# Kernel tuning notes

Measured on AMD Instinct MI355X. Metric: run time of the kernel, lower is better.

The kernel has to match this reference:

```python
import jax, jax.numpy as jnp
import numpy as np

B, N, NE = 4, 10000, 100000
D, S, H, T = 128, 64, 4, 128      # enc_dim, enc_s_dim, n_head, n_token
NS = D + S                        # GNN node_size = 192
EPS = 1e-5


def linear(x, w, b):
    return x @ w.T + b


def layer_norm(x, g, b):
    m = jnp.mean(x, -1, keepdims=True)
    v = jnp.mean((x - m) ** 2, -1, keepdims=True)
    return (x - m) * jax.lax.rsqrt(v + EPS) * g + b


def mha(q, k, v, wqkv, bqkv, wo, bo):
    # torch nn.MultiheadAttention, batch_first=True
    d = q.shape[-1]; hd = d // H
    wq, wk, wv = jnp.split(wqkv, 3, 0)
    bq, bk, bv = jnp.split(bqkv, 3, 0)
    def proj(x, w, bb):
        Bx, L, _ = x.shape
        return (x @ w.T + bb).reshape(Bx, L, H, hd)
    qh, kh, vh = proj(q, wq, bq), proj(k, wk, bk), proj(v, wv, bv)
    scores = jnp.einsum('bqhd,bkhd->bhqk', qh, kh) / jnp.sqrt(jnp.asarray(hd, q.dtype))
    att = jax.nn.softmax(scores, axis=-1)
    o = jnp.einsum('bhqk,bkhd->bqhd', att, vh).reshape(q.shape[0], q.shape[1], d)
    return o @ wo.T + bo


def smean(vals, idx, n):
    # scatter_mean over one batch element: vals (ne,f), idx (ne,)
    s = jax.ops.segment_sum(vals, idx, num_segments=n)
    c = jax.ops.segment_sum(jnp.ones(idx.shape, vals.dtype), idx, num_segments=n)
    return s / jnp.maximum(c, 1.0)[:, None]

_smean_b = jax.vmap(smean, in_axes=(0, 0, None))
_gather_b = jax.vmap(lambda v, i: v[i])


def setup_inputs():
    key = jax.random.key(0)
    ks = jax.random.split(key, 32)
    r = lambda i, shape: jax.random.normal(ks[i], shape, jnp.float32) * 0.02
    inp = {
        'V': jax.random.normal(ks[0], (B, N, D), jnp.float32),
        'E': jax.random.normal(ks[1], (B, NE, D), jnp.float32),
        'edges': jax.random.randint(ks[2], (B, NE, 2), 0, N),
        's_enc': jax.random.normal(ks[3], (B, N, S), jnp.float32),
        # GNN f_edge: Linear(512,128) SiLU Linear(128,128) LN(128)
        'fe_w1': r(4, (D, D + 2 * NS)), 'fe_b1': jnp.zeros(D),
        'fe_w2': r(5, (D, D)), 'fe_b2': jnp.zeros(D),
        'fe_g': jnp.ones(D), 'fe_be': jnp.zeros(D),
        # GNN f_node: Linear(320,128) SiLU Linear(128,128) LN(128)
        'fn_w1': r(6, (D, NS + D)), 'fn_b1': jnp.zeros(D),
        'fn_w2': r(7, (D, D)), 'fn_b2': jnp.zeros(D),
        'fn_g': jnp.ones(D), 'fn_be': jnp.zeros(D),
        'ln1_g': jnp.ones(D), 'ln1_b': jnp.zeros(D),
        'ln2_g': jnp.ones(D), 'ln2_b': jnp.zeros(D),
        'Q': jax.random.normal(ks[8], (T, D), jnp.float32),
        'a1_wqkv': r(9, (3 * D, D)), 'a1_bqkv': jnp.zeros(3 * D),
        'a1_wo': r(10, (D, D)), 'a1_bo': jnp.zeros(D),
        'a2_wqkv': r(11, (3 * D, D)), 'a2_bqkv': jnp.zeros(3 * D),
        'a2_wo': r(12, (D, D)), 'a2_bo': jnp.zeros(D),
        'a3_wqkv': r(13, (3 * D, D)), 'a3_bqkv': jnp.zeros(3 * D),
        'a3_wo': r(14, (D, D)), 'a3_bo': jnp.zeros(D),
        'ffn_w1': r(15, (2 * D, D)), 'ffn_b1': jnp.zeros(2 * D),
        'ffn_w2': r(16, (D, 2 * D)), 'ffn_b2': jnp.zeros(D),
    }
    return inp


def reference(V, E, edges, s_enc,
              fe_w1, fe_b1, fe_w2, fe_b2, fe_g, fe_be,
              fn_w1, fn_b1, fn_w2, fn_b2, fn_g, fn_be,
              ln1_g, ln1_b, ln2_g, ln2_b,
              Q, a1_wqkv, a1_bqkv, a1_wo, a1_bo,
              a2_wqkv, a2_bqkv, a2_wo, a2_bo,
              a3_wqkv, a3_bqkv, a3_wo, a3_bo,
              ffn_w1, ffn_b1, ffn_w2, ffn_b2):
    n = V.shape[1]
    V_in = jnp.concatenate([V, s_enc], -1)                  # (B,N,192)
    valid = jnp.all(edges >= 0, -1)                          # (B,NE)
    safe = jnp.clip(edges, 0, n - 1)
    senders = _gather_b(V_in, safe[..., 0])                  # (B,NE,192)
    receivers = _gather_b(V_in, safe[..., 1])
    edge_inpt = jnp.concatenate([senders, receivers, E], -1) # (B,NE,512)
    eh = jax.nn.silu(linear(edge_inpt, fe_w1, fe_b1))
    e_emb = layer_norm(linear(eh, fe_w2, fe_b2), fe_g, fe_be)
    e_emb = e_emb * valid[..., None].astype(e_emb.dtype)
    e0, e1 = jnp.split(e_emb, 2, -1)
    m0 = _smean_b(e0, safe[..., 0], n)
    m1 = _smean_b(e1, safe[..., 1], n)
    node_inpt = jnp.concatenate([V_in, m0, m1], -1)          # (B,N,320)
    nh = jax.nn.silu(linear(node_inpt, fn_w1, fn_b1))
    v_emb = layer_norm(linear(nh, fn_w2, fn_b2), fn_g, fn_be)
    E_out = E + e_emb
    V1 = V + v_emb
    # attention block
    W0 = layer_norm(V1, ln1_g, ln1_b)
    lq = jnp.broadcast_to(Q, (V.shape[0],) + Q.shape)
    W = mha(lq, W0, W0, a1_wqkv, a1_bqkv, a1_wo, a1_bo)
    W = mha(W, W, W, a2_wqkv, a2_bqkv, a2_wo, a2_bo)
    W = mha(W0, W, W, a3_wqkv, a3_bqkv, a3_wo, a3_bo)
    V2 = V1 + W
    # FFN block
    x = layer_norm(V2, ln2_g, ln2_b)
    V3 = V2 + linear(jax.nn.silu(linear(x, ffn_w1, ffn_b1)), ffn_w2, ffn_b2)
    return (V3, E_out)
```

## Files before the change

### kernel.cpp

```cpp
#include <hip/hip_runtime.h>
#include <hip/hip_bf16.h>

#define B_ 4
#define N_ 10000
#define NE_ 100000
#define D_ 128
#define S_ 64
#define H_ 4
#define T_ 128

typedef unsigned short u16;
typedef unsigned int u32;
typedef __attribute__((ext_vector_type(4))) float f4;
typedef __attribute__((ext_vector_type(8))) short s8;

#define DEVI static __device__ __forceinline__

DEVI float b2f(u16 u){ union{u32 i; float f;} v; v.i=((u32)u)<<16; return v.f; }
DEVI u16 f2b(float f){ union{float ff; u32 i;} v; v.ff=f; u32 i=v.i; return (u16)((i+0x7fffu+((i>>16)&1u))>>16); }
DEVI f4 mfma16(s8 a, s8 b, f4 c){ return __builtin_amdgcn_mfma_f32_16x16x32_bf16(a,b,c,0,0,0); }
DEVI float rsum16(float x){ x+=__shfl_xor(x,1); x+=__shfl_xor(x,2); x+=__shfl_xor(x,4); x+=__shfl_xor(x,8); return x; }
DEVI float silu_f(float v){ return v/(1.f+__expf(-v)); }
DEVI float nn(float v, float s){ return (v==v)? v : s; }
DEVI float lo2f(u32 u){ union{u32 i; float f;} v; v.i=u<<16; return v.f; }
// ... 7 lines not shown
  for (int i=0;i<4;i++){ u.t[i]=f2b(a[i]); u.t[4+i]=f2b(c[i]); }
  return u.v;
}
DEVI uint4 cvt8(const float* p){
  f4 a = *(const f4*)p;
  f4 c = *(const f4*)(p+4);
  union { u16 t[8]; uint4 v; } u;
  #pragma unroll
  for (int i=0;i<4;i++){ u.t[i]=f2b(a[i]); u.t[4+i]=f2b(c[i]); }
  return u.v;
}
DEVI uint4 cvt8nt(const float* p){
  f4 a = __builtin_nontemporal_load((const f4*)p);
  f4 c = __builtin_nontemporal_load((const f4*)(p+4));
  union { u16 t[8]; uint4 v; } u;
  #pragma unroll
  for (int i=0;i<4;i++){ u.t[i]=f2b(a[i]); u.t[4+i]=f2b(c[i]); }
  return u.v;
}

#define WO_FE1 0
#define WO_FE2 65536
#define WO_FN1 81920
#define WO_FN2 122880
#define WO_A1  139264
#define WO_A3  188416
#define WO_A3O 237568
#define WO_FF1 253952
#define WO_FF2 286720
#define WTOT   319488

__global__ __launch_bounds__(256) void k_cvtw(
  const float* __restrict__ s0, const float* __restrict__ s1,
  const float* __restrict__ s2, const float* __restrict__ s3,
  const float* __restrict__ s4, const float* __restrict__ s5,
  const float* __restrict__ s6, const float* __restrict__ s7,
  const float* __restrict__ s8v, u16* __restrict__ dst)
{
  int i = (blockIdx.x*256 + threadIdx.x)*8;
  if (i >= WTOT) return;
  const float* src; int off;
  if      (i < WO_FE2){ src=s0;  off=WO_FE1; }
  else if (i < WO_FN1){ src=s1;  off=WO_FE2; }
  else if (i < WO_FN2){ src=s2;  off=WO_FN1; }
  else if (i < WO_A1 ){ src=s3;  off=WO_FN2; }
  else if (i < WO_A3 ){ src=s4;  off=WO_A1;  }
  else if (i < WO_A3O){ src=s5;  off=WO_A3;  }
  else if (i < WO_FF1){ src=s6;  off=WO_A3O; }
  else if (i < WO_FF2){ src=s7;  off=WO_FF1; }
  else                { src=s8v; off=WO_FF2; }
  *(uint4*)(dst+i) = cvt8(src + (i-off));
}

__global__ __launch_bounds__(256,2) void k_edge(
  const float* __restrict__ V, const float* __restrict__ E, const int* __restrict__ edges,
  const float* __restrict__ senc,
  const u16* __restrict__ w1b, const float* __restrict__ b1,
  const u16* __restrict__ w2b, const float* __restrict__ b2,
  const float* __restrict__ lng, const float* __restrict__ lnb,
  float* __restrict__ m0s, float* __restrict__ m1s,
  float* __restrict__ c0s, float* __restrict__ c1s,
  float* __restrict__ Eout)
{
  __shared__ u16 X[64][520];
  __shared__ int gi0[64], gi1[64];
  __shared__ float fvalid[64];
  __shared__ float rsA[64][4], rsB[64][4];
  const int tid = threadIdx.x;
  const int el = tid>>2, part = tid&3;
  const int ge = blockIdx.x*64 + el;
  const int b = ge / NE_;
  const int2 ed = *(const int2*)(edges + (size_t)ge*2);
  const int i0 = min(max(ed.x,0),N_-1), i1 = min(max(ed.y,0),N_-1);
  if (part==0){
    gi0[el] = b*N_ + i0; gi1[el] = b*N_ + i1;
    fvalid[el] = (ed.x>=0 && ed.y>=0) ? 1.f : 0.f;
  }
  {
    const float* Vb = V + (size_t)b*N_*D_;
    const float* Sb = senc + (size_t)b*N_*S_;
    const float* Ep = E + (size_t)ge*D_;
    #pragma unroll
    for (int j=0;j<16;j++){
      int u = part + 4*j;
      if (u<48){
        const float* p;
        if (u<16)      p = Vb + (size_t)i0*D_ + u*8;
        else if (u<24) p = Sb + (size_t)i0*S_ + (u-16)*8;
        else if (u<40) p = Vb + (size_t)i1*D_ + (u-24)*8;
        else           p = Sb + (size_t)i1*S_ + (u-40)*8;
        *(uint4*)&X[el][u*8] = cvt8(p);
      } else {
        *(uint4*)&X[el][u*8] = cvt8nt(Ep + (u-48)*8);
      }
    }
  }
  __syncthreads();
  if (tid < 64){
    atomicAdd(&c0s[gi0[tid]], 1.f);
    atomicAdd(&c1s[gi1[tid]], 1.f);
  }
  const int lane = tid&63, w = tid>>6;
  const int l15 = lane&15, hi = lane>>4;
  const int colb = w*32;
  f4 acc[4][2];
  #pragma unroll
  for (int m=0;m<4;m++)
    #pragma unroll
    for (int tl=0;tl<2;tl++){ float bb=b1[colb+tl*16+l15]; acc[m][tl]=(f4){bb,bb,bb,bb}; }
  for (int kk=0;kk<16;kk++){
    s8 bfr[2];
    #pragma unroll
    for (int tl=0;tl<2;tl++)
      bfr[tl] = *(const s8*)(w1b + (size_t)(colb+tl*16+l15)*512 + kk*32 + hi*8);
    #pragma unroll
    for (int m=0;m<4;m++){
      s8 a = *(const s8*)&X[m*16+l15][kk*32 + hi*8];
      #pragma unroll
      for (int tl=0;tl<2;tl++) acc[m][tl] = mfma16(a, bfr[tl], acc[m][tl]);
    }
  }
  __syncthreads();
  #pragma unroll
  for (int m=0;m<4;m++)
    #pragma unroll
    for (int tl=0;tl<2;tl++)
      #pragma unroll
      for (int r=0;r<4;r++)
        X[m*16+hi*4+r][colb+tl*16+l15] = f2b(silu_f(acc[m][tl][r]));
  __syncthreads();
  f4 a2[4][2];
  #pragma unroll
  for (int m=0;m<4;m++)
    #pragma unroll
    for (int tl=0;tl<2;tl++){ float bb=b2[colb+tl*16+l15]; a2[m][tl]=(f4){bb,bb,bb,bb}; }
  #pragma unroll
  for (int kk=0;kk<4;kk++){
    s8 bfr[2];
    #pragma unroll
    for (int tl=0;tl<2;tl++)
      bfr[tl] = *(const s8*)(w2b + (size_t)(colb+tl*16+l15)*128 + kk*32 + hi*8);
    #pragma unroll
    for (int m=0;m<4;m++){
      s8 a = *(const s8*)&X[m*16+l15][kk*32 + hi*8];
      #pragma unroll
      for (int tl=0;tl<2;tl++) a2[m][tl] = mfma16(a, bfr[tl], a2[m][tl]);
    }
  }
  #pragma unroll
  for (int m=0;m<4;m++)
    #pragma unroll
    for (int r=0;r<4;r++){
      float ps=0.f, pq=0.f;
      #pragma unroll
      for (int tl=0;tl<2;tl++){ float v=a2[m][tl][r]; ps+=v; pq+=v*v; }
      ps=rsum16(ps); pq=rsum16(pq);
      if (l15==0){ int row=m*16+hi*4+r; rsA[row][w]=ps; rsB[row][w]=pq; }
    }
  __syncthreads();
  float gv[2], bev[2];
  #pragma unroll
  for (int tl=0;tl<2;tl++){ gv[tl]=lng[colb+tl*16+l15]; bev[tl]=lnb[colb+tl*16+l15]; }
  const int ge0 = blockIdx.x*64;
  #pragma unroll
  for (int m=0;m<4;m++)
    #pragma unroll
    for (int r=0;r<4;r++){
      const int row = m*16+hi*4+r;
      float s  = rsA[row][0]+rsA[row][1]+rsA[row][2]+rsA[row][3];
      float s2 = rsB[row][0]+rsB[row][1]+rsB[row][2]+rsB[row][3];
      const float mean = s*(1.f/128.f);
      const float rstd = rsqrtf(s2*(1.f/128.f) - mean*mean + 1e-5f);
      const float vm = fvalid[row];
      const int g0 = gi0[row], g1 = gi1[row];
      #pragma unroll
      for (int tl=0;tl<2;tl++){
        const int col = colb+tl*16+l15;
        float ev = ((a2[m][tl][r]-mean)*rstd*gv[tl] + bev[tl]) * vm;
        ev = nn(ev, 7e3f);
        if (col < 64) atomicAdd(m0s + (size_t)g0*64 + col, ev);
        else          atomicAdd(m1s + (size_t)g1*64 + (col-64), ev);
        float ef = b2f(X[row][384+col]);
        __builtin_nontemporal_store(ef + ev, Eout + (size_t)(ge0+row)*D_ + col);
      }
    }
}

__global__ __launch_bounds__(256,2) void k_node(
  const float* __restrict__ V, const float* __restrict__ senc,
  const float* __restrict__ m0s, const float* __restrict__ m1s,
  const float* __restrict__ c0s, const float* __restrict__ c1s,
  const u16* __restrict__ w1b, const float* __restrict__ b1,
  const u16* __restrict__ w2b, const float* __restrict__ b2,
  const float* __restrict__ lng, const float* __restrict__ lnb,
  const float* __restrict__ l1g, const float* __restrict__ l1b,
  u16* __restrict__ V1, u16* __restrict__ W0)
{
  __shared__ u16 X[64][328];
  __shared__ float rsA[64][4], rsB[64][4];
  const int tid=threadIdx.x, nl=tid>>2, part=tid&3;
  const int gn = blockIdx.x*64 + nl;
  const int b = gn / N_, n = gn - b*N_;
  {
    const float* Vp = V + ((size_t)b*N_ + n)*D_;
    const float* Sp = senc + ((size_t)b*N_ + n)*S_;
    #pragma unroll
    for (int j=0;j<6;j++){
      int u = part + 4*j;
      const float* p = (u<16)? Vp + u*8 : Sp + (u-16)*8;
      *(uint4*)&X[nl][u*8] = cvt8(p);
    }
    const float rc0 = 1.f/fmaxf(c0s[gn],1.f), rc1 = 1.f/fmaxf(c1s[gn],1.f);
    #pragma unroll
    for (int j=0;j<8;j++){
      int c = part*32 + j*4;
      const float* src = (c<64)? m0s + (size_t)gn*64 + c : m1s + (size_t)gn*64 + (c-64);
      float rr = (c<64)? rc0 : rc1;
      f4 mv = *(const f4*)src;
      u16 ov[4];
      #pragma unroll
      for (int i=0;i<4;i++) ov[i]=f2b(mv[i]*rr);
      uint2 pk; __builtin_memcpy(&pk, ov, 8);
      *(uint2*)&X[nl][192+c] = pk;
    }
  }
  __syncthreads();
  const int lane=tid&63, w=tid>>6, l15=lane&15, hi=lane>>4, colb=w*32;
  f4 acc[4][2];
  #pragma unroll
  for (int m=0;m<4;m++)
    #pragma unroll
    for (int tl=0;tl<2;tl++){ float bb=b1[colb+tl*16+l15]; acc[m][tl]=(f4){bb,bb,bb,bb}; }
  for (int kk=0;kk<10;kk++){
    s8 bfr[2];
    #pragma unroll
    for (int tl=0;tl<2;tl++)
      bfr[tl] = *(const s8*)(w1b + (size_t)(colb+tl*16+l15)*320 + kk*32 + hi*8);
    #pragma unroll
    for (int m=0;m<4;m++){
      s8 a = *(const s8*)&X[m*16+l15][kk*32+hi*8];
      #pragma unroll
      for (int tl=0;tl<2;tl++) acc[m][tl]=mfma16(a,bfr[tl],acc[m][tl]);
    }
  }
  __syncthreads();
  #pragma unroll
  for (int m=0;m<4;m++)
    #pragma unroll
    for (int tl=0;tl<2;tl++)
// ... 37 lines not shown
    gv[tl]=lng[col]; bev[tl]=lnb[col]; g1v[tl]=l1g[col]; b1v[tl]=l1b[col];
  }
  #pragma unroll
  for (int m=0;m<4;m++)
    #pragma unroll
    for (int r=0;r<4;r++){
      const int row=m*16+hi*4+r;
      float s  = rsA[row][0]+rsA[row][1]+rsA[row][2]+rsA[row][3];
      float s2 = rsB[row][0]+rsB[row][1]+rsB[row][2]+rsB[row][3];
      float mean=s*(1.f/128.f);
      float rstd=rsqrtf(s2*(1.f/128.f)-mean*mean+1e-5f);
      #pragma unroll
      for (int tl=0;tl<2;tl++){
        float ve=(a2[m][tl][r]-mean)*rstd*gv[tl]+bev[tl];
        a2[m][tl][r] = b2f(X[row][colb+tl*16+l15]) + ve;
      }
    }
  __syncthreads();
  #pragma unroll
  for (int m=0;m<4;m++)
    #pragma unroll
    for (int r=0;r<4;r++){
      float ps=0.f, pq=0.f;
      #pragma unroll
      for (int tl=0;tl<2;tl++){ float v=a2[m][tl][r]; ps+=v; pq+=v*v; }
      ps=rsum16(ps); pq=rsum16(pq);
      if (l15==0){ int row=m*16+hi*4+r; rsA[row][w]=ps; rsB[row][w]=pq; }
    }
  __syncthreads();
  #pragma unroll
  for (int m=0;m<4;m++)
    #pragma unroll
    for (int r=0;r<4;r++){
      const int row=m*16+hi*4+r;
      float sv  = rsA[row][0]+rsA[row][1]+rsA[row][2]+rsA[row][3];
      float sv2 = rsB[row][0]+rsB[row][1]+rsB[row][2]+rsB[row][3];
      float m2=sv*(1.f/128.f);
      float rs2=rsqrtf(sv2*(1.f/128.f)-m2*m2+1e-5f);
      #pragma unroll
      for (int tl=0;tl<2;tl++){
        int col=colb+tl*16+l15;
        float tmp=a2[m][tl][r];
        X[row][col]     = f2b(tmp);
        X[row][192+col] = f2b((tmp-m2)*rs2*g1v[tl]+b1v[tl]);
      }
    }
  __syncthreads();
  #pragma unroll
  for (int j=0;j<4;j++){
    int u=part+4*j;
    *(uint4*)(V1 + (size_t)gn*D_ + u*8) = *(const uint4*)&X[nl][u*8];
    *(uint4*)(W0 + (size_t)gn*D_ + u*8) = *(const uint4*)&X[nl][192 + u*8];
  }
}

__global__ __launch_bounds__(256) void k_qh1(
  const float* __restrict__ Q, const float* __restrict__ wqkv, const float* __restrict__ bqkv,
  u16* __restrict__ qh1)
{
  __shared__ u16 X[64][136];
  const int tid=threadIdx.x, nl=tid>>2, part=tid&3;
  const int q = blockIdx.x*64 + nl;
  #pragma unroll
  for (int j=0;j<4;j++){ int u=part+4*j; *(uint4*)&X[nl][u*8] = cvt8(Q + (size_t)q*D_ + u*8); }
  __syncthreads();
  const int lane=tid&63, w=tid>>6, l15=lane&15, hi=lane>>4, rw=w*16;
  f4 acc[8];
  #pragma unroll
  for (int t=0;t<8;t++){ float bb=bqkv[l15+16*t]; acc[t]=(f4){bb,bb,bb,bb}; }
  #pragma unroll
  for (int kk=0;kk<4;kk++){
    s8 a = *(const s8*)&X[rw+l15][kk*32+hi*8];
    #pragma unroll
    for (int t=0;t<8;t++){
      s8 bf = ldw8f(wqkv + (size_t)(t*16+l15)*D_ + kk*32+hi*8);
      acc[t]=mfma16(a,bf,acc[t]);
    }
  }
  __syncthreads();
  #pragma unroll
  for (int t=0;t<8;t++){
    #pragma unroll
    for (int r=0;r<4;r++) X[rw+hi*4+r][l15+16*t]=f2b(acc[t][r]);
  }
  __syncthreads();
  #pragma unroll
  for (int j=0;j<4;j++){
    int u=part+4*j, col0=u*8, h=col0>>5, d=col0&31;
    *(uint4*)(qh1 + ((size_t)h*T_ + q)*32 + d) = *(const uint4*)&X[nl][col0];
  }
}

__global__ __launch_bounds__(256,2) void k_kv1(
  const u16* __restrict__ W0, const u16* __restrict__ wqkvb, const float* __restrict__ bqkv,
  u16* __restrict__ kh1, u16* __restrict__ vh1)
{
  __shared__ u16 X[64][264];
  const int tid=threadIdx.x, nl=tid>>2, part=tid&3;
  const int gn = blockIdx.x*64 + nl;
  const int b = gn / N_, n = gn - b*N_;
  #pragma unroll
  for (int j=0;j<4;j++){ int u=part+4*j; *(uint4*)&X[nl][u*8] = *(const uint4*)(W0 + (size_t)gn*D_ + u*8); }
  __syncthreads();
  const int lane=tid&63, w=tid>>6, l15=lane&15, hi=lane>>4;
  const int colb = w*64;
  f4 acc[4][4];
  #pragma unroll
  for (int m=0;m<4;m++)
    #pragma unroll
    for (int tl=0;tl<4;tl++){ float bb=bqkv[128 + colb+tl*16+l15]; acc[m][tl]=(f4){bb,bb,bb,bb}; }
  #pragma unroll
  for (int kk=0;kk<4;kk++){
    s8 bfr[4];
    #pragma unroll
    for (int tl=0;tl<4;tl++)
      bfr[tl] = *(const s8*)(wqkvb + (size_t)(128 + colb+tl*16+l15)*D_ + kk*32+hi*8);
    #pragma unroll
    for (int m=0;m<4;m++){
      s8 a = *(const s8*)&X[m*16+l15][kk*32+hi*8];
      #pragma unroll
      for (int tl=0;tl<4;tl++) acc[m][tl]=mfma16(a,bfr[tl],acc[m][tl]);
    }
  }
  __syncthreads();
  #pragma unroll
  for (int m=0;m<4;m++)
    #pragma unroll
    for (int tl=0;tl<4;tl++)
      #pragma unroll
      for (int r=0;r<4;r++)
        X[m*16+hi*4+r][colb+tl*16+l15]=f2b(acc[m][tl][r]);
  __syncthreads();
  #pragma unroll
  for (int j=0;j<8;j++){
    int u=part+4*j, col0=u*8;
    u16* dst;
    if (col0<128){ int h=col0>>5, d=col0&31; dst = kh1 + ((size_t)(b*H_+h)*N_ + n)*32 + d; }
    else { int c2=col0-128; int h=c2>>5, d=c2&31; dst = vh1 + ((size_t)(b*H_+h)*N_ + n)*32 + d; }
    *(uint4*)dst = *(const uint4*)&X[nl][col0];
  }
}

#define NCH 20
#define CHK 512

__global__ __launch_bounds__(256,2) void k_mha1p(
  const u16* __restrict__ qh1, const u16* __restrict__ kh1, const u16* __restrict__ vh1,
  float* __restrict__ pm, float* __restrict__ pl, float* __restrict__ po)
{
  __shared__ u16 VT[32][72];
  __shared__ u16 P[4][32][72];
  const int bh = blockIdx.x / NCH, ch = blockIdx.x - bh*NCH;
  const int tid = threadIdx.x, w = tid>>6, lane = tid&63, l15=lane&15, hi=lane>>4;
  const int h = bh & 3;
  const int k0 = ch*CHK;
  const int nk = min(CHK, N_ - k0);
  const u16* Kb = kh1 + ((size_t)bh*N_ + k0)*32;
  const u16* Vb = vh1 + ((size_t)bh*N_ + k0)*32;
  s8 aq[2];
  #pragma unroll
  for (int qt=0;qt<2;qt++)
    aq[qt] = *(const s8*)(qh1 + ((size_t)h*T_ + w*32 + qt*16 + l15)*32 + hi*8);
  const float scale = 0.17677669529663687f;
  float m_reg[2][4], l_reg[2][4];
  f4 acc[2][2];
  #pragma unroll
  for (int qt=0;qt<2;qt++){
    #pragma unroll
    for (int r=0;r<4;r++){ m_reg[qt][r]=-1e30f; l_reg[qt][r]=0.f; }
    #pragma unroll
    for (int dt=0;dt<2;dt++) acc[qt][dt]=(f4){0.f,0.f,0.f,0.f};
  }
  const int ntile = (nk+63)>>6;
  for (int kt=0; kt<ntile; kt++){
    {
      int key = tid>>2, dseg = tid&3;
      int kg = kt*64 + key;
      uint4 v = (kg<nk)? *(const uint4*)(Vb + (size_t)kg*32 + dseg*8) : (uint4){0,0,0,0};
      const u16* vv = (const u16*)&v;
      #pragma unroll
      for (int i=0;i<8;i++) VT[dseg*8+i][key] = vv[i];
    }
    __syncthreads();
    f4 sa[2][4];
    #pragma unroll
    for (int kt4=0;kt4<4;kt4++){
      int key = kt*64 + kt4*16 + l15;
      int keyc = min(key, nk-1);
      s8 bk = *(const s8*)(Kb + (size_t)keyc*32 + hi*8);
      #pragma unroll
      for (int qt=0;qt<2;qt++)
        sa[qt][kt4] = mfma16(aq[qt], bk, (f4){0.f,0.f,0.f,0.f});
// ... 238 lines not shown
  {
    f4 acc[8];
    #pragma unroll
    for (int t=0;t<8;t++){ float bb=bo[l15+16*t]; acc[t]=(f4){bb,bb,bb,bb}; }
    #pragma unroll
    for (int kk=0;kk<4;kk++){
      s8 a = *(const s8*)&X[rw+l15][kk*32+hi*8];
      #pragma unroll
      for (int t=0;t<8;t++){
        s8 bf = ldw8f(wo + (size_t)(t*16+l15)*D_ + kk*32+hi*8);
        acc[t]=mfma16(a,bf,acc[t]);
      }
    }
    #pragma unroll
    for (int t=0;t<8;t++){
      #pragma unroll
      for (int r=0;r<4;r++) Y[rw+hi*4+r][l15+16*t]=f2b(acc[t][r]);
    }
  }
  __syncthreads();
  f4 a2[16];
  #pragma unroll
  for (int t=0;t<16;t++){ float bb=bqkv3[128 + l15+16*t]; a2[t]=(f4){bb,bb,bb,bb}; }
  #pragma unroll
  for (int kk=0;kk<4;kk++){
    s8 a = *(const s8*)&Y[rw+l15][kk*32+hi*8];
    #pragma unroll
    for (int t=0;t<16;t++){
      s8 bf = ldw8f(wqkv3 + (size_t)(128 + t*16+l15)*D_ + kk*32+hi*8);
      a2[t]=mfma16(a,bf,a2[t]);
    }
  }
  __syncthreads();
  #pragma unroll
  for (int t=0;t<16;t++){
    #pragma unroll
    for (int r=0;r<4;r++) Y[rw+hi*4+r][l15+16*t]=f2b(a2[t][r]);
  }
  __syncthreads();
  const int b=row>>7, q=row&127;
  #pragma unroll
  for (int j=0;j<4;j++){
    int u=part+4*j, col0=u*8, h=col0>>5, d=col0&31;
    *(uint4*)(kh3 + ((size_t)(b*H_+h)*T_ + q)*32 + d) = *(const uint4*)&Y[nl][col0];
  }
  #pragma unroll
  for (int cc=0;cc<32;cc++){
    int c2 = part*32 + cc;
    int h=c2>>5, d=c2&31;
    vh3T[((size_t)(b*H_+h)*32 + d)*T_ + q] = Y[nl][128+c2];
  }
}

__global__ __launch_bounds__(256,2) void k_mha3(
  const u16* __restrict__ W0, const u16* __restrict__ V1,
  const u16* __restrict__ wq3b, const float* __restrict__ bqkv3,
  const u16* __restrict__ kh3, const u16* __restrict__ vh3T,
  const u16* __restrict__ wo3b, const float* __restrict__ bo3,
  const float* __restrict__ l2g, const float* __restrict__ l2b,
  u16* __restrict__ V2, u16* __restrict__ XLN)
{
  __shared__ u16 Wt[64][136];
  __shared__ u16 Q3[64][136];
  __shared__ u16 P3[64][136];
  __shared__ float rsA[64][4], rsB[64][4];
  const int tid=threadIdx.x, nl=tid>>2, part=tid&3;
  const int b = blockIdx.x/157, tb = blockIdx.x - b*157;
  const int n0 = tb*64;
  {
    const int ns = min(n0+nl, N_-1);
    const u16* src = W0 + ((size_t)b*N_+ns)*D_;
    #pragma unroll
    for (int j=0;j<4;j++){ int u=part+4*j; *(uint4*)&Wt[nl][u*8] = *(const uint4*)(src+u*8); }
  }
  __syncthreads();
  const int lane=tid&63, w=tid>>6, l15=lane&15, hi=lane>>4;
  const int rw=w*16, colb=w*32;
  {
    f4 acc[4][2];
    #pragma unroll
    for (int m=0;m<4;m++)
      #pragma unroll
      for (int tl=0;tl<2;tl++){ float bb=bqkv3[colb+tl*16+l15]; acc[m][tl]=(f4){bb,bb,bb,bb}; }
    #pragma unroll
    for (int kk=0;kk<4;kk++){
      s8 bfr[2];
      #pragma unroll
      for (int tl=0;tl<2;tl++)
        bfr[tl] = *(const s8*)(wq3b + (size_t)(colb+tl*16+l15)*D_ + kk*32+hi*8);
      #pragma unroll
      for (int m=0;m<4;m++){
        s8 a = *(const s8*)&Wt[m*16+l15][kk*32+hi*8];
        #pragma unroll
        for (int tl=0;tl<2;tl++) acc[m][tl]=mfma16(a,bfr[tl],acc[m][tl]);
      }
    }
    #pragma unroll
    for (int m=0;m<4;m++)
      #pragma unroll
      for (int tl=0;tl<2;tl++)
        #pragma unroll
        for (int r=0;r<4;r++)
          Q3[m*16+hi*4+r][colb+tl*16+l15]=f2b(acc[m][tl][r]);
  }
  __syncthreads();
  const float scale=0.17677669529663687f;
  f4 oacc[8];
  #pragma unroll
  for (int t=0;t<8;t++) oacc[t]=(f4){0.f,0.f,0.f,0.f};
  #pragma unroll
  for (int h=0;h<H_;h++){
    f4 sa[8];
    #pragma unroll
// ... 45 lines not shown
    #pragma unroll
    for (int tl=0;tl<2;tl++){ float bb=bo3[colb+tl*16+l15]; a2[m][tl]=(f4){bb,bb,bb,bb}; }
  #pragma unroll
  for (int kk=0;kk<4;kk++){
    s8 bfr[2];
    #pragma unroll
    for (int tl=0;tl<2;tl++)
      bfr[tl] = *(const s8*)(wo3b + (size_t)(colb+tl*16+l15)*D_ + kk*32+hi*8);
    #pragma unroll
    for (int m=0;m<4;m++){
      s8 a = *(const s8*)&Q3[m*16+l15][kk*32+hi*8];
      #pragma unroll
      for (int tl=0;tl<2;tl++) a2[m][tl]=mfma16(a,bfr[tl],a2[m][tl]);
    }
  }
  #pragma unroll
  for (int m=0;m<4;m++)
    #pragma unroll
    for (int r=0;r<4;r++){
      const int row=m*16+hi*4+r;
      const int nr = min(n0+row, N_-1);
      const size_t gr=(size_t)b*N_+nr;
      float ps=0.f, pq=0.f;
      #pragma unroll
      for (int tl=0;tl<2;tl++){
        float tmp = b2f(V1[gr*D_ + colb+tl*16+l15]) + a2[m][tl][r];
        a2[m][tl][r]=tmp; ps+=tmp; pq+=tmp*tmp;
      }
      ps=rsum16(ps); pq=rsum16(pq);
      if (l15==0){ rsA[row][w]=ps; rsB[row][w]=pq; }
    }
  __syncthreads();
  float g2v[2],b2v[2];
  #pragma unroll
  for (int tl=0;tl<2;tl++){ g2v[tl]=l2g[colb+tl*16+l15]; b2v[tl]=l2b[colb+tl*16+l15]; }
  #pragma unroll
  for (int m=0;m<4;m++)
    #pragma unroll
    for (int r=0;r<4;r++){
      const int row=m*16+hi*4+r;
      float s  = rsA[row][0]+rsA[row][1]+rsA[row][2]+rsA[row][3];
      float s2 = rsB[row][0]+rsB[row][1]+rsB[row][2]+rsB[row][3];
      float mean=s*(1.f/128.f);
      float rstd=rsqrtf(s2*(1.f/128.f)-mean*mean+1e-5f);
      #pragma unroll
      for (int tl=0;tl<2;tl++){
        int col=colb+tl*16+l15;
        float tmp=a2[m][tl][r];
        P3[row][col]=f2b(tmp);
        Wt[row][col]=f2b((tmp-mean)*rstd*g2v[tl]+b2v[tl]);
      }
    }
  __syncthreads();
  if (n0+nl < N_){
    const size_t gd=(size_t)b*N_+n0+nl;
    #pragma unroll
    for (int j=0;j<4;j++){
      int u=part+4*j;
      *(uint4*)(V2 + gd*D_ + u*8) = *(const uint4*)&P3[nl][u*8];
      *(uint4*)(XLN + gd*D_ + u*8) = *(const uint4*)&Wt[nl][u*8];
    }
  }
}

__global__ __launch_bounds__(256,2) void k_ffn(
  const u16* __restrict__ XLN, const u16* __restrict__ V2,
  const u16* __restrict__ w1b, const float* __restrict__ b1,
  const u16* __restrict__ w2b, const float* __restrict__ b2,
  float* __restrict__ V3)
{
  __shared__ u16 Xs[64][136];
  __shared__ u16 Hs[64][136];
  const int tid=threadIdx.x, nl=tid>>2, part=tid&3;
  const size_t gn = (size_t)blockIdx.x*64 + nl;
  #pragma unroll
  for (int j=0;j<4;j++){ int u=part+4*j; *(uint4*)&Xs[nl][u*8] = *(const uint4*)(XLN + gn*D_ + u*8); }
  __syncthreads();
  const int lane=tid&63, w=tid>>6, l15=lane&15, hi=lane>>4, colb=w*32;
  f4 accf[4][2];
  #pragma unroll
  for (int m=0;m<4;m++)
    #pragma unroll
    for (int tl=0;tl<2;tl++){ float bb=b2[colb+tl*16+l15]; accf[m][tl]=(f4){bb,bb,bb,bb}; }
  for (int half=0;half<2;half++){
    f4 ah[4][2];
    #pragma unroll
    for (int m=0;m<4;m++)
      #pragma unroll
      for (int tl=0;tl<2;tl++){ float bb=b1[half*128+colb+tl*16+l15]; ah[m][tl]=(f4){bb,bb,bb,bb}; }
    #pragma unroll
    for (int kk=0;kk<4;kk++){
      s8 bfr[2];
      #pragma unroll
      for (int tl=0;tl<2;tl++)
        bfr[tl] = *(const s8*)(w1b + (size_t)(half*128+colb+tl*16+l15)*D_ + kk*32+hi*8);
      #pragma unroll
      for (int m=0;m<4;m++){
        s8 a = *(const s8*)&Xs[m*16+l15][kk*32+hi*8];
        #pragma unroll
        for (int tl=0;tl<2;tl++) ah[m][tl]=mfma16(a,bfr[tl],ah[m][tl]);
      }
    }
    __syncthreads();
    #pragma unroll
    for (int m=0;m<4;m++)
      #pragma unroll
      for (int tl=0;tl<2;tl++)
        #pragma unroll
        for (int r=0;r<4;r++)
          Hs[m*16+hi*4+r][colb+tl*16+l15]=f2b(silu_f(ah[m][tl][r]));
    __syncthreads();
    #pragma unroll
    for (int kk=0;kk<4;kk++){
      s8 bfr[2];
      #pragma unroll
      for (int tl=0;tl<2;tl++)
        bfr[tl] = *(const s8*)(w2b + (size_t)(colb+tl*16+l15)*256 + half*128 + kk*32+hi*8);
      #pragma unroll
      for (int m=0;m<4;m++){
        s8 a = *(const s8*)&Hs[m*16+l15][kk*32+hi*8];
        #pragma unroll
        for (int tl=0;tl<2;tl++) accf[m][tl]=mfma16(a,bfr[tl],accf[m][tl]);
      }
    }
  }
  #pragma unroll
  for (int m=0;m<4;m++)
    #pragma unroll
    for (int r=0;r<4;r++){
      const int row=m*16+hi*4+r;
      const size_t gr=(size_t)blockIdx.x*64+row;
      #pragma unroll
      for (int tl=0;tl<2;tl++){
        int col=colb+tl*16+l15;
        V3[gr*D_+col] = b2f(V2[gr*D_+col]) + accf[m][tl][r];
      }
    }
}

extern "C" void kernel_launch(void* const* d_in, const int* in_sizes, int n_in,
                              void* d_out, int out_size, void* d_ws, size_t ws_size,
                              hipStream_t stream)
{
  const float* V     = (const float*)d_in[0];
  const float* E     = (const float*)d_in[1];
  const int* edges   = (const int*)d_in[2];
  const float* senc  = (const float*)d_in[3];
  const float* fe_w1=(const float*)d_in[4];  const float* fe_b1=(const float*)d_in[5];
  const float* fe_w2=(const float*)d_in[6];  const float* fe_b2=(const float*)d_in[7];
  const float* fe_g =(const float*)d_in[8];  const float* fe_be=(const float*)d_in[9];
  const float* fn_w1=(const float*)d_in[10]; const float* fn_b1=(const float*)d_in[11];
  const float* fn_w2=(const float*)d_in[12]; const float* fn_b2=(const float*)d_in[13];
  const float* fn_g =(const float*)d_in[14]; const float* fn_be=(const float*)d_in[15];
  const float* ln1_g=(const float*)d_in[16]; const float* ln1_b=(const float*)d_in[17];
  const float* ln2_g=(const float*)d_in[18]; const float* ln2_b=(const float*)d_in[19];
  const float* Q    =(const float*)d_in[20];
  const float* a1_wqkv=(const float*)d_in[21]; const float* a1_bqkv=(const float*)d_in[22];
  const float* a1_wo=(const float*)d_in[23];   const float* a1_bo=(const float*)d_in[24];
  const float* a2_wqkv=(const float*)d_in[25]; const float* a2_bqkv=(const float*)d_in[26];
  const float* a2_wo=(const float*)d_in[27];   const float* a2_bo=(const float*)d_in[28];
  const float* a3_wqkv=(const float*)d_in[29]; const float* a3_bqkv=(const float*)d_in[30];
  const float* a3_wo=(const float*)d_in[31];   const float* a3_bo=(const float*)d_in[32];
  const float* ffn_w1=(const float*)d_in[33];  const float* ffn_b1=(const float*)d_in[34];
  const float* ffn_w2=(const float*)d_in[35];  const float* ffn_b2=(const float*)d_in[36];

  char* ws = (char*)d_ws;
  size_t off = 0;
  auto alloc = [&](size_t bytes)->void*{ void* p = ws + off; off += (bytes + 255) & ~(size_t)255; return p; };
  float* m0s = (float*)alloc((size_t)B_*N_*64*4);
  float* m1s = (float*)alloc((size_t)B_*N_*64*4);
  float* c0s = (float*)alloc((size_t)B_*N_*4);
  float* c1s = (float*)alloc((size_t)B_*N_*4);
  const size_t zero_bytes = off;
  u16* wcat = (u16*)alloc((size_t)WTOT*2);
  u16* V1  = (u16*)alloc((size_t)B_*N_*D_*2);
  u16* W0  = (u16*)alloc((size_t)B_*N_*D_*2);
  u16* kh1 = (u16*)alloc((size_t)B_*H_*N_*32*2);
  u16* vh1 = (u16*)alloc((size_t)B_*H_*N_*32*2);
  u16* qh1 = (u16*)alloc((size_t)H_*T_*32*2);
  float* o1 = (float*)alloc((size_t)B_*T_*D_*4);
  u16* qh2 = (u16*)alloc((size_t)B_*H_*T_*32*2);
  u16* kh2 = (u16*)alloc((size_t)B_*H_*T_*32*2);
  u16* vh2 = (u16*)alloc((size_t)B_*H_*T_*32*2);
  float* o2 = (float*)alloc((size_t)B_*T_*D_*4);
  u16* kh3 = (u16*)alloc((size_t)B_*H_*T_*32*2);
  u16* vh3T= (u16*)alloc((size_t)B_*H_*32*T_*2);
  u16* V2  = (u16*)alloc((size_t)B_*N_*D_*2);
  u16* XLN = (u16*)alloc((size_t)B_*N_*D_*2);
  float* pmw = (float*)alloc((size_t)B_*H_*NCH*128*4);
  float* plw = (float*)alloc((size_t)B_*H_*NCH*128*4);
  float* pow_ = (float*)alloc((size_t)B_*H_*NCH*128*32*4);
  if (ws_size < off) return;

  u16* w_fe1 = wcat + WO_FE1;
  u16* w_fe2 = wcat + WO_FE2;
  u16* w_fn1 = wcat + WO_FN1;
  u16* w_fn2 = wcat + WO_FN2;
  u16* w_a1  = wcat + WO_A1;
  u16* w_a3  = wcat + WO_A3;
  u16* w_a3o = wcat + WO_A3O;
  u16* w_ff1 = wcat + WO_FF1;
  u16* w_ff2 = wcat + WO_FF2;

  float* outp = (float*)d_out;
  float* V3out = outp;
  float* Eout  = outp + (size_t)B_*N_*D_;

  hipMemsetAsync(d_ws, 0, zero_bytes, stream);
  k_cvtw<<<(WTOT/8+255)/256,256,0,stream>>>(fe_w1,fe_w2,fn_w1,fn_w2,a1_wqkv,a3_wqkv,a3_wo,
                                            ffn_w1,ffn_w2, wcat);
  k_edge<<<(B_*NE_)/64,256,0,stream>>>(V,E,edges,senc, w_fe1,fe_b1, w_fe2,fe_b2, fe_g,fe_be,
                                       m0s,m1s,c0s,c1s, Eout);
  k_node<<<(B_*N_)/64,256,0,stream>>>(V,senc,m0s,m1s,c0s,c1s, w_fn1,fn_b1, w_fn2,fn_b2,
                                      fn_g,fn_be, ln1_g,ln1_b, V1,W0);
  k_qh1<<<T_/64,256,0,stream>>>(Q, a1_wqkv, a1_bqkv, qh1);
  k_kv1<<<(B_*N_)/64,256,0,stream>>>(W0, w_a1, a1_bqkv, kh1, vh1);
  k_mha1p<<<B_*H_*NCH,256,0,stream>>>(qh1,kh1,vh1, pmw,plw,pow_);
  k_mha1c<<<(B_*H_*T_*32)/256,256,0,stream>>>(pmw,plw,pow_, o1);
  k_att12<<<(B_*T_)/64,256,0,stream>>>(o1, a1_wo, a1_bo, a2_wqkv, a2_bqkv, qh2,kh2,vh2);
  k_mha2<<<(B_*H_*T_)/4,256,0,stream>>>(qh2,kh2,vh2,o2);
  k_att23<<<(B_*T_)/64,256,0,stream>>>(o2, a2_wo, a2_bo, a3_wqkv, a3_bqkv, kh3, vh3T);
  k_mha3<<<B_*157,256,0,stream>>>(W0,V1, w_a3,a3_bqkv, kh3,vh3T, w_a3o,a3_bo,
                                  ln2_g,ln2_b, V2,XLN);
  k_ffn<<<(B_*N_)/64,256,0,stream>>>(XLN,V2, w_ff1,ffn_b1, w_ff2,ffn_b2, V3out);
}
```

Measured before the change: 627.4 us.

## Widen edge kernel to 8 waves, fuse KV projection into node and FFN into mha3

```diff
diff --git a/kernel.cpp b/kernel.cpp
--- a/kernel.cpp
+++ b/kernel.cpp
@@ -83,7 +83,7 @@
   *(uint4*)(dst+i) = cvt8(src + (i-off));
 }
 
-__global__ __launch_bounds__(256,2) void k_edge(
+__global__ __launch_bounds__(512,4) void k_edge(
   const float* __restrict__ V, const float* __restrict__ E, const int* __restrict__ edges,
   const float* __restrict__ senc,
   const u16* __restrict__ w1b, const float* __restrict__ b1,
@@ -96,9 +96,9 @@
   __shared__ u16 X[64][520];
   __shared__ int gi0[64], gi1[64];
   __shared__ float fvalid[64];
-  __shared__ float rsA[64][4], rsB[64][4];
+  __shared__ float rsA[64][8], rsB[64][8];
   const int tid = threadIdx.x;
-  const int el = tid>>2, part = tid&3;
+  const int el = tid>>3, part = tid&7;
   const int ge = blockIdx.x*64 + el;
   const int b = ge / NE_;
   const int2 ed = *(const int2*)(edges + (size_t)ge*2);
@@ -112,8 +112,8 @@
     const float* Sb = senc + (size_t)b*N_*S_;
     const float* Ep = E + (size_t)ge*D_;
     #pragma unroll
-    for (int j=0;j<16;j++){
-      int u = part + 4*j;
+    for (int j=0;j<8;j++){
+      int u = part + 8*j;
       if (u<48){
         const float* p;
         if (u<16)      p = Vb + (size_t)i0*D_ + u*8;
@@ -133,91 +133,70 @@
   }
   const int lane = tid&63, w = tid>>6;
   const int l15 = lane&15, hi = lane>>4;
-  const int colb = w*32;
-  f4 acc[4][2];
-  #pragma unroll
-  for (int m=0;m<4;m++)
-    #pragma unroll
-    for (int tl=0;tl<2;tl++){ float bb=b1[colb+tl*16+l15]; acc[m][tl]=(f4){bb,bb,bb,bb}; }
+  const int colb = w*16;
+  f4 acc[4];
+  #pragma unroll
+  for (int m=0;m<4;m++){ float bb=b1[colb+l15]; acc[m]=(f4){bb,bb,bb,bb}; }
   for (int kk=0;kk<16;kk++){
-    s8 bfr[2];
-    #pragma unroll
-    for (int tl=0;tl<2;tl++)
-      bfr[tl] = *(const s8*)(w1b + (size_t)(colb+tl*16+l15)*512 + kk*32 + hi*8);
+    s8 bfr = *(const s8*)(w1b + (size_t)(colb+l15)*512 + kk*32 + hi*8);
     #pragma unroll
     for (int m=0;m<4;m++){
       s8 a = *(const s8*)&X[m*16+l15][kk*32 + hi*8];
-      #pragma unroll
-      for (int tl=0;tl<2;tl++) acc[m][tl] = mfma16(a, bfr[tl], acc[m][tl]);
-    }
-  }
-  __syncthreads();
-  #pragma unroll
-  for (int m=0;m<4;m++)
-    #pragma unroll
-    for (int tl=0;tl<2;tl++)
-      #pragma unroll
-      for (int r=0;r<4;r++)
-        X[m*16+hi*4+r][colb+tl*16+l15] = f2b(silu_f(acc[m][tl][r]));
-  __syncthreads();
-  f4 a2[4][2];
-  #pragma unroll
-  for (int m=0;m<4;m++)
-    #pragma unroll
-    for (int tl=0;tl<2;tl++){ float bb=b2[colb+tl*16+l15]; a2[m][tl]=(f4){bb,bb,bb,bb}; }
+      acc[m] = mfma16(a, bfr, acc[m]);
+    }
+  }
+  __syncthreads();
+  #pragma unroll
+  for (int m=0;m<4;m++)
+    #pragma unroll
+    for (int r=0;r<4;r++)
+      X[m*16+hi*4+r][colb+l15] = f2b(silu_f(acc[m][r]));
+  __syncthreads();
+  f4 a2[4];
+  #pragma unroll
+  for (int m=0;m<4;m++){ float bb=b2[colb+l15]; a2[m]=(f4){bb,bb,bb,bb}; }
   #pragma unroll
   for (int kk=0;kk<4;kk++){
-    s8 bfr[2];
-    #pragma unroll
-    for (int tl=0;tl<2;tl++)
-      bfr[tl] = *(const s8*)(w2b + (size_t)(colb+tl*16+l15)*128 + kk*32 + hi*8);
+    s8 bfr = *(const s8*)(w2b + (size_t)(colb+l15)*128 + kk*32 + hi*8);
     #pragma unroll
     for (int m=0;m<4;m++){
       s8 a = *(const s8*)&X[m*16+l15][kk*32 + hi*8];
-      #pragma unroll
-      for (int tl=0;tl<2;tl++) a2[m][tl] = mfma16(a, bfr[tl], a2[m][tl]);
+      a2[m] = mfma16(a, bfr, a2[m]);
     }
   }
   #pragma unroll
   for (int m=0;m<4;m++)
     #pragma unroll
     for (int r=0;r<4;r++){
-      float ps=0.f, pq=0.f;
-      #pragma unroll
-      for (int tl=0;tl<2;tl++){ float v=a2[m][tl][r]; ps+=v; pq+=v*v; }
-      ps=rsum16(ps); pq=rsum16(pq);
+      float v=a2[m][r];
+      float ps=rsum16(v), pq=rsum16(v*v);
       if (l15==0){ int row=m*16+hi*4+r; rsA[row][w]=ps; rsB[row][w]=pq; }
     }
   __syncthreads();
-  float gv[2], bev[2];
-  #pragma unroll
-  for (int tl=0;tl<2;tl++){ gv[tl]=lng[colb+tl*16+l15]; bev[tl]=lnb[colb+tl*16+l15]; }
+  const float gv=lng[colb+l15], bev=lnb[colb+l15];
   const int ge0 = blockIdx.x*64;
   #pragma unroll
   for (int m=0;m<4;m++)
     #pragma unroll
     for (int r=0;r<4;r++){
       const int row = m*16+hi*4+r;
-      float s  = rsA[row][0]+rsA[row][1]+rsA[row][2]+rsA[row][3];
-      float s2 = rsB[row][0]+rsB[row][1]+rsB[row][2]+rsB[row][3];
+      float s=0.f, s2=0.f;
+      #pragma unroll
+      for (int ww=0;ww<8;ww++){ s+=rsA[row][ww]; s2+=rsB[row][ww]; }
       const float mean = s*(1.f/128.f);
       const float rstd = rsqrtf(s2*(1.f/128.f) - mean*mean + 1e-5f);
       const float vm = fvalid[row];
-      const int g0 = gi0[row], g1 = gi1[row];
-      #pragma unroll
-      for (int tl=0;tl<2;tl++){
-        const int col = colb+tl*16+l15;
-        float ev = ((a2[m][tl][r]-mean)*rstd*gv[tl] + bev[tl]) * vm;
-        ev = nn(ev, 7e3f);
-        if (col < 64) atomicAdd(m0s + (size_t)g0*64 + col, ev);
-        else          atomicAdd(m1s + (size_t)g1*64 + (col-64), ev);
-        float ef = b2f(X[row][384+col]);
-        __builtin_nontemporal_store(ef + ev, Eout + (size_t)(ge0+row)*D_ + col);
-      }
-    }
-}
-
-__global__ __launch_bounds__(256,2) void k_node(
+      const int col = colb+l15;
+      float ev = ((a2[m][r]-mean)*rstd*gv + bev) * vm;
+      ev = nn(ev, 7e3f);
+      if (col < 64) atomicAdd(m0s + (size_t)gi0[row]*64 + col, ev);
+      else          atomicAdd(m1s + (size_t)gi1[row]*64 + (col-64), ev);
+      float ef = b2f(X[row][384+col]);
+      __builtin_nontemporal_store(ef + ev, Eout + (size_t)(ge0+row)*D_ + col);
+    }
+}
+
+__global__ __launch_bounds__(256,2) void k_nodekv(
   const float* __restrict__ V, const float* __restrict__ senc,
   const float* __restrict__ m0s, const float* __restrict__ m1s,
   const float* __restrict__ c0s, const float* __restrict__ c1s,
@@ -225,7 +204,9 @@
   const u16* __restrict__ w2b, const float* __restrict__ b2,
   const float* __restrict__ lng, const float* __restrict__ lnb,
   const float* __restrict__ l1g, const float* __restrict__ l1b,
-  u16* __restrict__ V1, u16* __restrict__ W0)
+  const u16* __restrict__ wqkvb, const float* __restrict__ bqkv,
+  u16* __restrict__ V1, u16* __restrict__ W0,
+  u16* __restrict__ kh1, u16* __restrict__ vh1)
 {
   __shared__ u16 X[64][328];
   __shared__ float rsA[64][4], rsB[64][4];
@@ -369,74 +350,23 @@
     *(uint4*)(V1 + (size_t)gn*D_ + u*8) = *(const uint4*)&X[nl][u*8];
     *(uint4*)(W0 + (size_t)gn*D_ + u*8) = *(const uint4*)&X[nl][192 + u*8];
   }
-}
-
-__global__ __launch_bounds__(256) void k_qh1(
-  const float* __restrict__ Q, const float* __restrict__ wqkv, const float* __restrict__ bqkv,
-  u16* __restrict__ qh1)
-{
-  __shared__ u16 X[64][136];
-  const int tid=threadIdx.x, nl=tid>>2, part=tid&3;
-  const int q = blockIdx.x*64 + nl;
-  #pragma unroll
-  for (int j=0;j<4;j++){ int u=part+4*j; *(uint4*)&X[nl][u*8] = cvt8(Q + (size_t)q*D_ + u*8); }
-  __syncthreads();
-  const int lane=tid&63, w=tid>>6, l15=lane&15, hi=lane>>4, rw=w*16;
-  f4 acc[8];
-  #pragma unroll
-  for (int t=0;t<8;t++){ float bb=bqkv[l15+16*t]; acc[t]=(f4){bb,bb,bb,bb}; }
-  #pragma unroll
-  for (int kk=0;kk<4;kk++){
-    s8 a = *(const s8*)&X[rw+l15][kk*32+hi*8];
-    #pragma unroll
-    for (int t=0;t<8;t++){
-      s8 bf = ldw8f(wqkv + (size_t)(t*16+l15)*D_ + kk*32+hi*8);
-      acc[t]=mfma16(a,bf,acc[t]);
-    }
-  }
-  __syncthreads();
-  #pragma unroll
-  for (int t=0;t<8;t++){
-    #pragma unroll
-    for (int r=0;r<4;r++) X[rw+hi*4+r][l15+16*t]=f2b(acc[t][r]);
-  }
-  __syncthreads();
-  #pragma unroll
-  for (int j=0;j<4;j++){
-    int u=part+4*j, col0=u*8, h=col0>>5, d=col0&31;
-    *(uint4*)(qh1 + ((size_t)h*T_ + q)*32 + d) = *(const uint4*)&X[nl][col0];
-  }
-}
-
-__global__ __launch_bounds__(256,2) void k_kv1(
-  const u16* __restrict__ W0, const u16* __restrict__ wqkvb, const float* __restrict__ bqkv,
-  u16* __restrict__ kh1, u16* __restrict__ vh1)
-{
-  __shared__ u16 X[64][264];
-  const int tid=threadIdx.x, nl=tid>>2, part=tid&3;
-  const int gn = blockIdx.x*64 + nl;
-  const int b = gn / N_, n = gn - b*N_;
-  #pragma unroll
-  for (int j=0;j<4;j++){ int u=part+4*j; *(uint4*)&X[nl][u*8] = *(const uint4*)(W0 + (size_t)gn*D_ + u*8); }
-  __syncthreads();
-  const int lane=tid&63, w=tid>>6, l15=lane&15, hi=lane>>4;
-  const int colb = w*64;
-  f4 acc[4][4];
-  #pragma unroll
-  for (int m=0;m<4;m++)
-    #pragma unroll
-    for (int tl=0;tl<4;tl++){ float bb=bqkv[128 + colb+tl*16+l15]; acc[m][tl]=(f4){bb,bb,bb,bb}; }
+  const int colb2 = w*64;
+  f4 acck[4][4];
+  #pragma unroll
+  for (int m=0;m<4;m++)
+    #pragma unroll
+    for (int tl=0;tl<4;tl++){ float bb=bqkv[128 + colb2+tl*16+l15]; acck[m][tl]=(f4){bb,bb,bb,bb}; }
   #pragma unroll
   for (int kk=0;kk<4;kk++){
     s8 bfr[4];
     #pragma unroll
     for (int tl=0;tl<4;tl++)
-      bfr[tl] = *(const s8*)(wqkvb + (size_t)(128 + colb+tl*16+l15)*D_ + kk*32+hi*8);
+      bfr[tl] = *(const s8*)(wqkvb + (size_t)(128 + colb2+tl*16+l15)*D_ + kk*32+hi*8);
     #pragma unroll
     for (int m=0;m<4;m++){
-      s8 a = *(const s8*)&X[m*16+l15][kk*32+hi*8];
-      #pragma unroll
-      for (int tl=0;tl<4;tl++) acc[m][tl]=mfma16(a,bfr[tl],acc[m][tl]);
+      s8 a = *(const s8*)&X[m*16+l15][192 + kk*32+hi*8];
+      #pragma unroll
+      for (int tl=0;tl<4;tl++) acck[m][tl]=mfma16(a,bfr[tl],acck[m][tl]);
     }
   }
   __syncthreads();
@@ -446,7 +376,7 @@
     for (int tl=0;tl<4;tl++)
       #pragma unroll
       for (int r=0;r<4;r++)
-        X[m*16+hi*4+r][colb+tl*16+l15]=f2b(acc[m][tl][r]);
+        X[m*16+hi*4+r][colb2+tl*16+l15]=f2b(acck[m][tl][r]);
   __syncthreads();
   #pragma unroll
   for (int j=0;j<8;j++){
@@ -455,6 +385,43 @@
     if (col0<128){ int h=col0>>5, d=col0&31; dst = kh1 + ((size_t)(b*H_+h)*N_ + n)*32 + d; }
     else { int c2=col0-128; int h=c2>>5, d=c2&31; dst = vh1 + ((size_t)(b*H_+h)*N_ + n)*32 + d; }
     *(uint4*)dst = *(const uint4*)&X[nl][col0];
+  }
+}
+
+__global__ __launch_bounds__(256) void k_qh1(
+  const float* __restrict__ Q, const float* __restrict__ wqkv, const float* __restrict__ bqkv,
+  u16* __restrict__ qh1)
+{
+  __shared__ u16 X[64][136];
+  const int tid=threadIdx.x, nl=tid>>2, part=tid&3;
+  const int q = blockIdx.x*64 + nl;
+  #pragma unroll
+  for (int j=0;j<4;j++){ int u=part+4*j; *(uint4*)&X[nl][u*8] = cvt8(Q + (size_t)q*D_ + u*8); }
+  __syncthreads();
+  const int lane=tid&63, w=tid>>6, l15=lane&15, hi=lane>>4, rw=w*16;
+  f4 acc[8];
+  #pragma unroll
+  for (int t=0;t<8;t++){ float bb=bqkv[l15+16*t]; acc[t]=(f4){bb,bb,bb,bb}; }
+  #pragma unroll
+  for (int kk=0;kk<4;kk++){
+    s8 a = *(const s8*)&X[rw+l15][kk*32+hi*8];
+    #pragma unroll
+    for (int t=0;t<8;t++){
+      s8 bf = ldw8f(wqkv + (size_t)(t*16+l15)*D_ + kk*32+hi*8);
+      acc[t]=mfma16(a,bf,acc[t]);
+    }
+  }
+  __syncthreads();
+  #pragma unroll
+  for (int t=0;t<8;t++){
+    #pragma unroll
+    for (int r=0;r<4;r++) X[rw+hi*4+r][l15+16*t]=f2b(acc[t][r]);
+  }
+  __syncthreads();
+  #pragma unroll
+  for (int j=0;j<4;j++){
+    int u=part+4*j, col0=u*8, h=col0>>5, d=col0&31;
+    *(uint4*)(qh1 + ((size_t)h*T_ + q)*32 + d) = *(const uint4*)&X[nl][col0];
   }
 }
 
@@ -799,13 +766,15 @@
   }
 }
 
-__global__ __launch_bounds__(256,2) void k_mha3(
+__global__ __launch_bounds__(256,2) void k_mha3f(
   const u16* __restrict__ W0, const u16* __restrict__ V1,
   const u16* __restrict__ wq3b, const float* __restrict__ bqkv3,
   const u16* __restrict__ kh3, const u16* __restrict__ vh3T,
   const u16* __restrict__ wo3b, const float* __restrict__ bo3,
   const float* __restrict__ l2g, const float* __restrict__ l2b,
-  u16* __restrict__ V2, u16* __restrict__ XLN)
+  const u16* __restrict__ fw1b, const float* __restrict__ fb1,
+  const u16* __restrict__ fw2b, const float* __restrict__ fb2,
+  float* __restrict__ V3)
 {
   __shared__ u16 Wt[64][136];
   __shared__ u16 Q3[64][136];
@@ -957,51 +926,26 @@
       }
     }
   __syncthreads();
-  if (n0+nl < N_){
-    const size_t gd=(size_t)b*N_+n0+nl;
-    #pragma unroll
-    for (int j=0;j<4;j++){
-      int u=part+4*j;
-      *(uint4*)(V2 + gd*D_ + u*8) = *(const uint4*)&P3[nl][u*8];
-      *(uint4*)(XLN + gd*D_ + u*8) = *(const uint4*)&Wt[nl][u*8];
-    }
-  }
-}
-
-__global__ __launch_bounds__(256,2) void k_ffn(
-  const u16* __restrict__ XLN, const u16* __restrict__ V2,
-  const u16* __restrict__ w1b, const float* __restrict__ b1,
-  const u16* __restrict__ w2b, const float* __restrict__ b2,
-  float* __restrict__ V3)
-{
-  __shared__ u16 Xs[64][136];
-  __shared__ u16 Hs[64][136];
-  const int tid=threadIdx.x, nl=tid>>2, part=tid&3;
-  const size_t gn = (size_t)blockIdx.x*64 + nl;
-  #pragma unroll
-  for (int j=0;j<4;j++){ int u=part+4*j; *(uint4*)&Xs[nl][u*8] = *(const uint4*)(XLN + gn*D_ + u*8); }
-  __syncthreads();
-  const int lane=tid&63, w=tid>>6, l15=lane&15, hi=lane>>4, colb=w*32;
   f4 accf[4][2];
   #pragma unroll
   for (int m=0;m<4;m++)
     #pragma unroll
-    for (int tl=0;tl<2;tl++){ float bb=b2[colb+tl*16+l15]; accf[m][tl]=(f4){bb,bb,bb,bb}; }
+    for (int tl=0;tl<2;tl++){ float bb=fb2[colb+tl*16+l15]; accf[m][tl]=(f4){bb,bb,bb,bb}; }
   for (int half=0;half<2;half++){
     f4 ah[4][2];
     #pragma unroll
     for (int m=0;m<4;m++)
       #pragma unroll
-      for (int tl=0;tl<2;tl++){ float bb=b1[half*128+colb+tl*16+l15]; ah[m][tl]=(f4){bb,bb,bb,bb}; }
+      for (int tl=0;tl<2;tl++){ float bb=fb1[half*128+colb+tl*16+l15]; ah[m][tl]=(f4){bb,bb,bb,bb}; }
     #pragma unroll
     for (int kk=0;kk<4;kk++){
       s8 bfr[2];
       #pragma unroll
       for (int tl=0;tl<2;tl++)
-        bfr[tl] = *(const s8*)(w1b + (size_t)(half*128+colb+tl*16+l15)*D_ + kk*32+hi*8);
+        bfr[tl] = *(const s8*)(fw1b + (size_t)(half*128+colb+tl*16+l15)*D_ + kk*32+hi*8);
       #pragma unroll
       for (int m=0;m<4;m++){
-        s8 a = *(const s8*)&Xs[m*16+l15][kk*32+hi*8];
+        s8 a = *(const s8*)&Wt[m*16+l15][kk*32+hi*8];
         #pragma unroll
         for (int tl=0;tl<2;tl++) ah[m][tl]=mfma16(a,bfr[tl],ah[m][tl]);
       }
@@ -1013,17 +957,17 @@
       for (int tl=0;tl<2;tl++)
         #pragma unroll
         for (int r=0;r<4;r++)
-          Hs[m*16+hi*4+r][colb+tl*16+l15]=f2b(silu_f(ah[m][tl][r]));
+          Q3[m*16+hi*4+r][colb+tl*16+l15]=f2b(silu_f(ah[m][tl][r]));
     __syncthreads();
     #pragma unroll
     for (int kk=0;kk<4;kk++){
       s8 bfr[2];
       #pragma unroll
       for (int tl=0;tl<2;tl++)
-        bfr[tl] = *(const s8*)(w2b + (size_t)(colb+tl*16+l15)*256 + half*128 + kk*32+hi*8);
+        bfr[tl] = *(const s8*)(fw2b + (size_t)(colb+tl*16+l15)*256 + half*128 + kk*32+hi*8);
       #pragma unroll
       for (int m=0;m<4;m++){
-        s8 a = *(const s8*)&Hs[m*16+l15][kk*32+hi*8];
+        s8 a = *(const s8*)&Q3[m*16+l15][kk*32+hi*8];
         #pragma unroll
         for (int tl=0;tl<2;tl++) accf[m][tl]=mfma16(a,bfr[tl],accf[m][tl]);
       }
@@ -1034,11 +978,13 @@
     #pragma unroll
     for (int r=0;r<4;r++){
       const int row=m*16+hi*4+r;
-      const size_t gr=(size_t)blockIdx.x*64+row;
-      #pragma unroll
-      for (int tl=0;tl<2;tl++){
-        int col=colb+tl*16+l15;
-        V3[gr*D_+col] = b2f(V2[gr*D_+col]) + accf[m][tl][r];
+      if (n0+row < N_){
+        const size_t gr=(size_t)b*N_+n0+row;
+        #pragma unroll
+        for (int tl=0;tl<2;tl++){
+          int col=colb+tl*16+l15;
+          V3[gr*D_+col] = b2f(P3[row][col]) + accf[m][tl][r];
+        }
       }
     }
 }
@@ -1090,8 +1036,6 @@
   float* o2 = (float*)alloc((size_t)B_*T_*D_*4);
   u16* kh3 = (u16*)alloc((size_t)B_*H_*T_*32*2);
   u16* vh3T= (u16*)alloc((size_t)B_*H_*32*T_*2);
-  u16* V2  = (u16*)alloc((size_t)B_*N_*D_*2);
-  u16* XLN = (u16*)alloc((size_t)B_*N_*D_*2);
   float* pmw = (float*)alloc((size_t)B_*H_*NCH*128*4);
   float* plw = (float*)alloc((size_t)B_*H_*NCH*128*4);
   float* pow_ = (float*)alloc((size_t)B_*H_*NCH*128*32*4);
@@ -1114,18 +1058,17 @@
   hipMemsetAsync(d_ws, 0, zero_bytes, stream);
   k_cvtw<<<(WTOT/8+255)/256,256,0,stream>>>(fe_w1,fe_w2,fn_w1,fn_w2,a1_wqkv,a3_wqkv,a3_wo,
                                             ffn_w1,ffn_w2, wcat);
-  k_edge<<<(B_*NE_)/64,256,0,stream>>>(V,E,edges,senc, w_fe1,fe_b1, w_fe2,fe_b2, fe_g,fe_be,
+  k_edge<<<(B_*NE_)/64,512,0,stream>>>(V,E,edges,senc, w_fe1,fe_b1, w_fe2,fe_b2, fe_g,fe_be,
                                        m0s,m1s,c0s,c1s, Eout);
-  k_node<<<(B_*N_)/64,256,0,stream>>>(V,senc,m0s,m1s,c0s,c1s, w_fn1,fn_b1, w_fn2,fn_b2,
-                                      fn_g,fn_be, ln1_g,ln1_b, V1,W0);
+  k_nodekv<<<(B_*N_)/64,256,0,stream>>>(V,senc,m0s,m1s,c0s,c1s, w_fn1,fn_b1, w_fn2,fn_b2,
+                                        fn_g,fn_be, ln1_g,ln1_b, w_a1,a1_bqkv,
+                                        V1,W0, kh1,vh1);
   k_qh1<<<T_/64,256,0,stream>>>(Q, a1_wqkv, a1_bqkv, qh1);
-  k_kv1<<<(B_*N_)/64,256,0,stream>>>(W0, w_a1, a1_bqkv, kh1, vh1);
   k_mha1p<<<B_*H_*NCH,256,0,stream>>>(qh1,kh1,vh1, pmw,plw,pow_);
   k_mha1c<<<(B_*H_*T_*32)/256,256,0,stream>>>(pmw,plw,pow_, o1);
   k_att12<<<(B_*T_)/64,256,0,stream>>>(o1, a1_wo, a1_bo, a2_wqkv, a2_bqkv, qh2,kh2,vh2);
   k_mha2<<<(B_*H_*T_)/4,256,0,stream>>>(qh2,kh2,vh2,o2);
   k_att23<<<(B_*T_)/64,256,0,stream>>>(o2, a2_wo, a2_bo, a3_wqkv, a3_bqkv, kh3, vh3T);
-  k_mha3<<<B_*157,256,0,stream>>>(W0,V1, w_a3,a3_bqkv, kh3,vh3T, w_a3o,a3_bo,
-                                  ln2_g,ln2_b, V2,XLN);
-  k_ffn<<<(B_*N_)/64,256,0,stream>>>(XLN,V2, w_ff1,ffn_b1, w_ff2,ffn_b2, V3out);
-}
+  k_mha3f<<<B_*157,256,0,stream>>>(W0,V1, w_a3,a3_bqkv, kh3,vh3T, w_a3o,a3_bo,
+                                   ln2_g,ln2_b, w_ff1,ffn_b1, w_ff2,ffn_b2, V3out);
+}
```

Result: no change. 619.7 us (-1.2%).
